# Performance work log

Hardware: AMD Instinct MI355X
Metric: run time of the kernel (lower is better)

The kernel has to match this reference:

```python
import jax, jax.numpy as jnp
import numpy as np

B, L, C = 4, 2048, 1024
H = 16
D = C // H  # 64
MAX_SCALE_MUL = float(np.log(100.0))


def setup_inputs() -> dict:
    key = jax.random.key(0)
    ks = jax.random.split(key, 8)
    x = jax.random.normal(ks[0], (B, L, C), dtype=jnp.float32)
    attn_bias = jax.random.normal(ks[1], (1, H, L, L), dtype=jnp.float32) * 0.02
    # nn.Linear(C, 3C, bias=False): weight [3C, C], init ~ U(-1/sqrt(C), 1/sqrt(C))
    lim = 1.0 / np.sqrt(C)
    W_qkv = jax.random.uniform(ks[2], (3 * C, C), minval=-lim, maxval=lim, dtype=jnp.float32)
    q_bias = jnp.zeros((C,), dtype=jnp.float32)
    v_bias = jnp.zeros((C,), dtype=jnp.float32)
    scale_mul_log = jnp.full((1, H, 1, 1), np.log(4.0), dtype=jnp.float32)
    W_proj = jax.random.uniform(ks[3], (C, C), minval=-lim, maxval=lim, dtype=jnp.float32)
    b_proj = jax.random.uniform(ks[4], (C,), minval=-lim, maxval=lim, dtype=jnp.float32)
    return {"x": x, "attn_bias": attn_bias, "W_qkv": W_qkv, "q_bias": q_bias,
            "v_bias": v_bias, "scale_mul_log": scale_mul_log,
            "W_proj": W_proj, "b_proj": b_proj}


def reference(x, attn_bias, W_qkv, q_bias, v_bias, scale_mul_log, W_proj, b_proj):
    Bc, Lc, Cc = x.shape
    qkv_bias = jnp.concatenate([q_bias, jnp.zeros_like(q_bias), v_bias])
    qkv = x @ W_qkv.T + qkv_bias                      # [B, L, 3C]
    qkv = qkv.reshape(Bc, Lc, 3, H, D)
    q, k, v = jnp.moveaxis(qkv, 2, 0)                 # each [B, L, H, D]
    q = jnp.swapaxes(q, 1, 2)                         # [B, H, L, D]
    k = jnp.swapaxes(k, 1, 2)
    v = jnp.swapaxes(v, 1, 2)
    # L2-norm cosine attention with learned per-head scale
    scale_mul = jnp.exp(jnp.minimum(scale_mul_log, MAX_SCALE_MUL))  # [1, H, 1, 1]
    q = q / jnp.linalg.norm(q, axis=-1, keepdims=True).clip(1e-12) * scale_mul
    k = k / jnp.linalg.norm(k, axis=-1, keepdims=True).clip(1e-12)
    attn = jnp.einsum('bhqd,bhkd->bhqk', q, k) + attn_bias
    attn = jax.nn.softmax(attn, axis=-1)
    out = jnp.einsum('bhqk,bhkd->bhqd', attn, v)      # [B, H, L, D]
    out = jnp.swapaxes(out, 1, 2).reshape(Bc, Lc, Cc)
    return out @ W_proj.T + b_proj
```

## Files before the change

### kernel.cpp

```cpp
#include <hip/hip_runtime.h>
#include <cstdint>
#include <cstddef>

#define BATCH 4
#define SEQ   2048
#define CMOD  1024
#define NH    16
#define DH    64
#define LOG100 4.6051701859880914f
#define LOG2E  1.4426950408889634f

typedef __attribute__((ext_vector_type(8))) short bf16x8;
typedef __attribute__((ext_vector_type(4))) float f32x4;
typedef __attribute__((ext_vector_type(16))) float f32x16;

__device__ __forceinline__ float u32lo_f(uint32_t u) {
    union { uint32_t i; float f; } x; x.i = u << 16; return x.f;
}
__device__ __forceinline__ float u32hi_f(uint32_t u) {
    union { uint32_t i; float f; } x; x.i = u & 0xFFFF0000u; return x.f;
}
__device__ __forceinline__ uint16_t f2bf(float f) {
    union { float f; uint32_t i; } x; x.f = f;
    uint32_t u = x.i;
    return (uint16_t)((u + 0x7FFFu + ((u >> 16) & 1u)) >> 16);
}
__device__ __forceinline__ float exp2_fast(float x) {
    float r; asm("v_exp_f32 %0, %1" : "=v"(r) : "v"(x)); return r;
}
__device__ __forceinline__ uint32_t cvt_pk_bf16(float lo, float hi) {
    uint32_t r;
    asm("v_cvt_pk_bf16_f32 %0, %1, %2" : "=v"(r) : "v"(lo), "v"(hi));
    return r;
}
__device__ __forceinline__ void p32swap(uint32_t& x, uint32_t& y) {
#if __has_builtin(__builtin_amdgcn_permlane32_swap)
    auto r = __builtin_amdgcn_permlane32_swap(x, y, false, false);
    x = r[0]; y = r[1];
#else
    asm volatile("v_permlane32_swap_b32 %0, %1\n\ts_nop 1" : "+v"(x), "+v"(y));
#endif
}

__device__ __forceinline__ void gload_lds16(const void* g, void* l) {
    __builtin_amdgcn_global_load_lds(
        (const __attribute__((address_space(1))) uint32_t*)g,
        (__attribute__((address_space(3))) uint32_t*)l,
        16, 0, 0);
}

__global__ __launch_bounds__(256) void cvt_kernel(const float* __restrict__ in,
                                                  uint16_t* __restrict__ out, int n) {
    int i = (blockIdx.x * 256 + threadIdx.x) * 4;
    if (i >= n) return;
    float4 f = *(const float4*)(in + i);
    ushort4 o;
    o.x = f2bf(f.x); o.y = f2bf(f.y); o.z = f2bf(f.z); o.w = f2bf(f.w);
    *(ushort4*)(out + i) = o;
}

__global__ __launch_bounds__(256) void gemm_bt_kernel(
    const uint16_t* __restrict__ A, const uint16_t* __restrict__ B,
    int M, int N, int K, int mode,
    uint16_t* __restrict__ qb, uint16_t* __restrict__ kb, uint16_t* __restrict__ vtb,
    const float* __restrict__ q_bias, const float* __restrict__ v_bias,
    const float* __restrict__ scale_mul_log,
    float* __restrict__ outp, const float* __restrict__ b_proj)
{
    __shared__ __align__(16) uint16_t As[128 * 32];
    __shared__ __align__(16) uint16_t Bs[128 * 32];
    const int t = threadIdx.x;
    const int wave = t >> 6, lane = t & 63;
    const int g = lane >> 4, c16 = lane & 15;
    const int m0 = blockIdx.x * 128, n0 = blockIdx.y * 128;
    const int wm = (wave >> 1) * 64, wn = (wave & 1) * 64;

    f32x4 acc[4][4];
#pragma unroll
    for (int mt = 0; mt < 4; mt++)
#pragma unroll
        for (int nt = 0; nt < 4; nt++) acc[mt][nt] = (f32x4){0.f, 0.f, 0.f, 0.f};

    for (int k0 = 0; k0 < K; k0 += 32) {
        __syncthreads();
#pragma unroll
        for (int i = 0; i < 2; i++) {
            int cc = i * 256 + t;
            int row = cc >> 2, col = (cc & 3) * 8;
            gload_lds16(A + (size_t)(m0 + row) * K + k0 + col, &As[cc * 8]);
            gload_lds16(B + (size_t)(n0 + row) * K + k0 + col, &Bs[cc * 8]);
        }
        __syncthreads();
        bf16x8 af[4], bfv[4];
#pragma unroll
        for (int mt = 0; mt < 4; mt++)
            af[mt] = *(const bf16x8*)&As[(wm + mt * 16 + c16) * 32 + g * 8];
#pragma unroll
        for (int nt = 0; nt < 4; nt++)
            bfv[nt] = *(const bf16x8*)&Bs[(wn + nt * 16 + c16) * 32 + g * 8];
#pragma unroll
        for (int mt = 0; mt < 4; mt++)
#pragma unroll
            for (int nt = 0; nt < 4; nt++)
                acc[mt][nt] = __builtin_amdgcn_mfma_f32_16x16x32_bf16(af[mt], bfv[nt], acc[mt][nt], 0, 0, 0);
    }

    if (mode == 0) {
        const int colbase = n0 + wn;
        const int tt = colbase >> 10;
        const int cc0 = colbase & 1023;
        const int hh = cc0 >> 6;
        float qmul = 1.0f;
        if (tt == 0) qmul = __expf(fminf(scale_mul_log[hh], LOG100)) * LOG2E;
#pragma unroll
        for (int mt = 0; mt < 4; mt++) {
            float vals[4][4];
            float n2[4] = {0.f, 0.f, 0.f, 0.f};
#pragma unroll
            for (int nt = 0; nt < 4; nt++) {
                const int ci = cc0 + nt * 16 + c16;
                float badd = 0.f;
                if (tt == 0) badd = q_bias[ci];
                else if (tt == 2) badd = v_bias[ci];
#pragma unroll
                for (int r = 0; r < 4; r++) {
                    float v = acc[mt][nt][r] + badd;
                    vals[nt][r] = v;
                    n2[r] += v * v;
                }
            }
            float rs[4];
            if (tt < 2) {
#pragma unroll
                for (int r = 0; r < 4; r++) {
                    float s = n2[r];
                    s += __shfl_xor(s, 1, 64);
                    s += __shfl_xor(s, 2, 64);
                    s += __shfl_xor(s, 4, 64);
                    s += __shfl_xor(s, 8, 64);
                    rs[r] = qmul / fmaxf(sqrtf(s), 1e-12f);
                }
            } else {
#pragma unroll
                for (int r = 0; r < 4; r++) rs[r] = 1.0f;
            }
#pragma unroll
            for (int nt = 0; nt < 4; nt++) {
                const int dd = (cc0 + nt * 16 + c16) & 63;
#pragma unroll
                for (int r = 0; r < 4; r++) {
                    const int row = m0 + wm + mt * 16 + g * 4 + r;
                    const int bb = row >> 11, ll = row & 2047;
                    const size_t bhx = (size_t)bb * NH + hh;
                    const uint16_t val = f2bf(vals[nt][r] * rs[r]);
                    if (tt < 2) {
                        size_t addr = ((bhx * 64 + (ll >> 5)) * 4 + (dd >> 4)) * 512
                                      + ((dd >> 3) & 1) * 256 + (ll & 31) * 8 + (dd & 7);
                        if (tt == 0) qb[addr] = val; else kb[addr] = val;
                    } else {
                        size_t addr = ((bhx * 64 + (ll >> 5)) * 4 + (dd >> 5) * 2 + ((ll >> 4) & 1)) * 512
                                      + (((ll >> 3) & 1) * 32 + (dd & 31)) * 8 + (ll & 7);
                        vtb[addr] = val;
                    }
                }
            }
        }
    } else {
#pragma unroll
        for (int mt = 0; mt < 4; mt++)
#pragma unroll
            for (int nt = 0; nt < 4; nt++)
#pragma unroll
                for (int r = 0; r < 4; r++) {
                    int row = m0 + wm + mt * 16 + g * 4 + r;
                    int col = n0 + wn + nt * 16 + c16;
                    outp[(size_t)row * N + col] = acc[mt][nt][r] + b_proj[col];
                }
    }
}

__global__ __launch_bounds__(256) void attn_kernel(
    const uint16_t* __restrict__ qfrag, const uint16_t* __restrict__ kfrag,
    const uint16_t* __restrict__ vfrag, const float* __restrict__ bias,
    uint16_t* __restrict__ ob)
{
    __shared__ __align__(16) uint16_t KsL[2 * 4 * 4 * 512];
    __shared__ __align__(16) uint16_t VsL[2 * 4 * 4 * 512];
    __shared__ __align__(16) uint2    Bsh[2 * 512];

    const int t = threadIdx.x;
    const int w = t >> 6, lane = t & 63;
    const int c32 = lane & 31, hi = lane >> 5;

    const int h = blockIdx.x >> 5;
    const int qt = blockIdx.x & 31;
    const int q0 = qt * 64;
    const size_t bh = (size_t)w * NH + h;

    bf16x8 qf[2][4];
#pragma unroll
    for (int qg = 0; qg < 2; qg++)
#pragma unroll
        for (int s = 0; s < 4; s++)
            qf[qg][s] = *(const bf16x8*)(qfrag +
                ((bh * 64 + (size_t)(qt * 2 + qg)) * 4 + s) * 512 + hi * 256 + c32 * 8);

    auto stage = [&](int tl, int buf) {
        const uint16_t* kp = kfrag + ((bh * 64 + (size_t)tl) * 4) * 512 + lane * 8;
        const uint16_t* vp = vfrag + ((bh * 64 + (size_t)tl) * 4) * 512 + lane * 8;
#pragma unroll
        for (int s = 0; s < 4; s++)
            gload_lds16(kp + s * 512, &KsL[((buf * 4 + w) * 4 + s) * 512 + lane * 8]);
#pragma unroll
        for (int s = 0; s < 4; s++)
            gload_lds16(vp + s * 512, &VsL[((buf * 4 + w) * 4 + s) * 512 + lane * 8]);
    };

    const int brow = t >> 2, kpart = t & 3;
    const float* bgl = bias + ((size_t)h * SEQ + q0 + brow) * SEQ + kpart * 8;
    const int u0 = kpart * 128 + (brow >> 5) * 64 + (brow & 31);

    auto writeBsh = [&](int buf, float4 a, float4 b) {
        Bsh[buf * 512 + u0] =
            make_uint2(cvt_pk_bf16(a.x * LOG2E, a.y * LOG2E),
                       cvt_pk_bf16(a.z * LOG2E, a.w * LOG2E));
        Bsh[buf * 512 + u0 + 32] =
            make_uint2(cvt_pk_bf16(b.x * LOG2E, b.y * LOG2E),
                       cvt_pk_bf16(b.z * LOG2E, b.w * LOG2E));
    };

    f32x16 accO[2][2];
#pragma unroll
    for (int qg = 0; qg < 2; qg++)
#pragma unroll
        for (int db = 0; db < 2; db++)
#pragma unroll
            for (int i = 0; i < 16; i++) accO[qg][db][i] = 0.f;
    float lrun[2] = {0.f, 0.f};

    float4 a0 = *(const float4*)(bgl);
    float4 a1 = *(const float4*)(bgl + 4);
    float4 br0 = *(const float4*)(bgl + 32);
    float4 br1 = *(const float4*)(bgl + 36);
    stage(0, 0);
    writeBsh(0, a0, a1);
    asm volatile("s_waitcnt lgkmcnt(0)" ::: "memory");
    __builtin_amdgcn_s_barrier();

    for (int it = 0; it < 64; ++it) {
        const int cur = it & 1;
        if (it < 63) {
            const int nb = cur ^ 1;
            writeBsh(nb, br0, br1);
            int n2 = it + 2; if (n2 > 63) n2 = 63;
            br0 = *(const float4*)(bgl + n2 * 32);
            br1 = *(const float4*)(bgl + n2 * 32 + 4);
            stage(it + 1, nb);
            asm volatile("s_waitcnt vmcnt(10)" ::: "memory");
        } else {
            asm volatile("s_waitcnt vmcnt(0)" ::: "memory");
        }

        bf16x8 kf[4], vf[4];
#pragma unroll
        for (int s = 0; s < 4; s++)
            kf[s] = *(const bf16x8*)&KsL[((cur * 4 + w) * 4 + s) * 512 + lane * 8];
#pragma unroll
        for (int s = 0; s < 4; s++)
            vf[s] = *(const bf16x8*)&VsL[((cur * 4 + w) * 4 + s) * 512 + lane * 8];

#pragma unroll
        for (int qg = 0; qg < 2; qg++) {
            f32x16 S;
#pragma unroll
            for (int i = 0; i < 16; i++) S[i] = 0.f;
            __builtin_amdgcn_s_setprio(1);
#pragma unroll
            for (int s = 0; s < 4; s++)
                S = __builtin_amdgcn_mfma_f32_32x32x16_bf16(kf[s], qf[qg][s], S, 0, 0, 0);
            __builtin_amdgcn_s_setprio(0);

            float p[16];
            float lp = 0.f;
#pragma unroll
            for (int tt = 0; tt < 4; tt++) {
                uint2 uu = Bsh[cur * 512 + tt * 128 + qg * 64 + hi * 32 + c32];
                p[tt * 4 + 0] = exp2_fast(S[tt * 4 + 0] + u32lo_f(uu.x));
                p[tt * 4 + 1] = exp2_fast(S[tt * 4 + 1] + u32hi_f(uu.x));
                p[tt * 4 + 2] = exp2_fast(S[tt * 4 + 2] + u32lo_f(uu.y));
                p[tt * 4 + 3] = exp2_fast(S[tt * 4 + 3] + u32hi_f(uu.y));
                lp += (p[tt * 4 + 0] + p[tt * 4 + 1]) + (p[tt * 4 + 2] + p[tt * 4 + 3]);
            }
            lrun[qg] += lp;

            bf16x8 pa[2];
#pragma unroll
            for (int cp = 0; cp < 2; cp++) {
                uint32_t X0 = cvt_pk_bf16(p[8 * cp + 0], p[8 * cp + 1]);
                uint32_t X1 = cvt_pk_bf16(p[8 * cp + 2], p[8 * cp + 3]);
                uint32_t Y0 = cvt_pk_bf16(p[8 * cp + 4], p[8 * cp + 5]);
                uint32_t Y1 = cvt_pk_bf16(p[8 * cp + 6], p[8 * cp + 7]);
                p32swap(X0, Y0);
                p32swap(X1, Y1);
                union { uint32_t u[4]; bf16x8 v; } pu;
                pu.u[0] = X0; pu.u[1] = X1; pu.u[2] = Y0; pu.u[3] = Y1;
                pa[cp] = pu.v;
            }

            __builtin_amdgcn_s_setprio(1);
#pragma unroll
            for (int c = 0; c < 2; c++)
#pragma unroll
                for (int db = 0; db < 2; db++)
                    accO[qg][db] = __builtin_amdgcn_mfma_f32_32x32x16_bf16(
                        pa[c], vf[db * 2 + c], accO[qg][db], 0, 0, 0);
            __builtin_amdgcn_s_setprio(0);
        }

        asm volatile("s_waitcnt lgkmcnt(0)" ::: "memory");
        __builtin_amdgcn_s_barrier();
    }

#pragma unroll
    for (int qg = 0; qg < 2; qg++) {
        float s = lrun[qg] + __shfl_xor(lrun[qg], 32, 64);
        float inv = 1.0f / s;
        float linv[16];
#pragma unroll
        for (int r = 0; r < 16; r++)
            linv[r] = __shfl(inv, (r & 3) + 8 * (r >> 2) + 4 * hi, 64);
#pragma unroll
        for (int r = 0; r < 16; r++) {
            int rowq = (r & 3) + 8 * (r >> 2) + 4 * hi;
            size_t rowbase = ((size_t)w * SEQ + q0 + qg * 32 + rowq) * CMOD + h * DH;
            ob[rowbase + c32]      = f2bf(accO[qg][0][r] * linv[r]);
            ob[rowbase + 32 + c32] = f2bf(accO[qg][1][r] * linv[r]);
        }
    }
}

extern "C" void kernel_launch(void* const* d_in, const int* in_sizes, int n_in,
                              void* d_out, int out_size, void* d_ws, size_t ws_size,
                              hipStream_t stream) {
    const float* x             = (const float*)d_in[0];
    const float* attn_bias     = (const float*)d_in[1];
    const float* W_qkv         = (const float*)d_in[2];
    const float* q_bias        = (const float*)d_in[3];
    const float* v_bias        = (const float*)d_in[4];
    const float* scale_mul_log = (const float*)d_in[5];
    const float* W_proj        = (const float*)d_in[6];
    const float* b_proj        = (const float*)d_in[7];
    float* out = (float*)d_out;

    uint8_t* ws = (uint8_t*)d_ws;
    size_t off = 0;
    auto alloc = [&](size_t bytes) { uint8_t* p = ws + off; off += (bytes + 255) & ~(size_t)255; return p; };
    uint16_t* xb     = (uint16_t*)alloc((size_t)8192 * 1024 * 2);
    uint16_t* wqkvb  = (uint16_t*)alloc((size_t)3072 * 1024 * 2);
    uint16_t* wprojb = (uint16_t*)alloc((size_t)1024 * 1024 * 2);
    uint16_t* qb     = (uint16_t*)alloc((size_t)BATCH * NH * SEQ * DH * 2);
    uint16_t* kb     = (uint16_t*)alloc((size_t)BATCH * NH * SEQ * DH * 2);
    uint16_t* vtb    = (uint16_t*)alloc((size_t)BATCH * NH * SEQ * DH * 2);
    uint16_t* ob     = (uint16_t*)alloc((size_t)BATCH * SEQ * CMOD * 2);
    (void)ws_size;

    cvt_kernel<<<8192, 256, 0, stream>>>(x, xb, 8388608);
    cvt_kernel<<<3072, 256, 0, stream>>>(W_qkv, wqkvb, 3145728);
    cvt_kernel<<<1024, 256, 0, stream>>>(W_proj, wprojb, 1048576);

    dim3 g1(64, 24);
    gemm_bt_kernel<<<g1, 256, 0, stream>>>(xb, wqkvb, 8192, 3072, 1024, 0,
                                           qb, kb, vtb, q_bias, v_bias, scale_mul_log,
                                           nullptr, nullptr);

    attn_kernel<<<512, 256, 0, stream>>>(qb, kb, vtb, attn_bias, ob);

    dim3 g3(64, 8);
    gemm_bt_kernel<<<g3, 256, 0, stream>>>(ob, wprojb, 8192, 1024, 1024, 1,
                                           nullptr, nullptr, nullptr, nullptr, nullptr, nullptr,
                                           out, b_proj);
}
```

Before: 304.8 us.

## Split attention work across eight waves per block, one query half each

Doubles the attention block to 512 threads. Each wave now handles one batch and a 32-row query half instead of both halves, and the K and V staging is split between the two groups of waves. The bias load per thread is halved, and explicit vmcnt/lgkmcnt waits and setprio are replaced with __syncthreads. The aim is more waves in flight to hide latency and less register use per wave, at the cost of larger blocks and coarser synchronisation.

```diff
diff --git a/kernel.cpp b/kernel.cpp
--- a/kernel.cpp
+++ b/kernel.cpp
@@ -179,7 +179,7 @@
     }
 }
 
-__global__ __launch_bounds__(256) void attn_kernel(
+__global__ __launch_bounds__(512, 4) void attn_kernel(
     const uint16_t* __restrict__ qfrag, const uint16_t* __restrict__ kfrag,
     const uint16_t* __restrict__ vfrag, const float* __restrict__ bias,
     uint16_t* __restrict__ ob)
@@ -189,153 +189,131 @@
     __shared__ __align__(16) uint2    Bsh[2 * 512];
 
     const int t = threadIdx.x;
-    const int w = t >> 6, lane = t & 63;
+    const int w8 = t >> 6, lane = t & 63;
+    const int b = w8 & 3, qhalf = w8 >> 2;
     const int c32 = lane & 31, hi = lane >> 5;
 
     const int h = blockIdx.x >> 5;
     const int qt = blockIdx.x & 31;
-    const int q0 = qt * 64;
-    const size_t bh = (size_t)w * NH + h;
-
-    bf16x8 qf[2][4];
-#pragma unroll
-    for (int qg = 0; qg < 2; qg++)
-#pragma unroll
-        for (int s = 0; s < 4; s++)
-            qf[qg][s] = *(const bf16x8*)(qfrag +
-                ((bh * 64 + (size_t)(qt * 2 + qg)) * 4 + s) * 512 + hi * 256 + c32 * 8);
+    const int q0w = qt * 64 + qhalf * 32;
+    const size_t bh = (size_t)b * NH + h;
+
+    bf16x8 qf[4];
+#pragma unroll
+    for (int s = 0; s < 4; s++)
+        qf[s] = *(const bf16x8*)(qfrag +
+            ((bh * 64 + (size_t)(qt * 2 + qhalf)) * 4 + s) * 512 + hi * 256 + c32 * 8);
 
     auto stage = [&](int tl, int buf) {
-        const uint16_t* kp = kfrag + ((bh * 64 + (size_t)tl) * 4) * 512 + lane * 8;
-        const uint16_t* vp = vfrag + ((bh * 64 + (size_t)tl) * 4) * 512 + lane * 8;
-#pragma unroll
-        for (int s = 0; s < 4; s++)
-            gload_lds16(kp + s * 512, &KsL[((buf * 4 + w) * 4 + s) * 512 + lane * 8]);
-#pragma unroll
-        for (int s = 0; s < 4; s++)
-            gload_lds16(vp + s * 512, &VsL[((buf * 4 + w) * 4 + s) * 512 + lane * 8]);
+        if (w8 < 4) {
+            const uint16_t* kp = kfrag + (((size_t)w8 * NH + h) * 64 + tl) * 4 * 512 + lane * 8;
+#pragma unroll
+            for (int s = 0; s < 4; s++)
+                gload_lds16(kp + s * 512, &KsL[((buf * 4 + w8) * 4 + s) * 512 + lane * 8]);
+        } else {
+            const int bb = w8 - 4;
+            const uint16_t* vp = vfrag + (((size_t)bb * NH + h) * 64 + tl) * 4 * 512 + lane * 8;
+#pragma unroll
+            for (int s = 0; s < 4; s++)
+                gload_lds16(vp + s * 512, &VsL[((buf * 4 + bb) * 4 + s) * 512 + lane * 8]);
+        }
     };
 
-    const int brow = t >> 2, kpart = t & 3;
-    const float* bgl = bias + ((size_t)h * SEQ + q0 + brow) * SEQ + kpart * 8;
-    const int u0 = kpart * 128 + (brow >> 5) * 64 + (brow & 31);
-
-    auto writeBsh = [&](int buf, float4 a, float4 b) {
+    const int brow = t >> 3, kch = t & 7;
+    const float* bgl = bias + ((size_t)h * SEQ + qt * 64 + brow) * SEQ + kch * 4;
+    const int u0 = (kch >> 1) * 128 + (brow >> 5) * 64 + (kch & 1) * 32 + (brow & 31);
+
+    auto writeBsh = [&](int buf, float4 a) {
         Bsh[buf * 512 + u0] =
             make_uint2(cvt_pk_bf16(a.x * LOG2E, a.y * LOG2E),
                        cvt_pk_bf16(a.z * LOG2E, a.w * LOG2E));
-        Bsh[buf * 512 + u0 + 32] =
-            make_uint2(cvt_pk_bf16(b.x * LOG2E, b.y * LOG2E),
-                       cvt_pk_bf16(b.z * LOG2E, b.w * LOG2E));
     };
 
-    f32x16 accO[2][2];
-#pragma unroll
-    for (int qg = 0; qg < 2; qg++)
-#pragma unroll
-        for (int db = 0; db < 2; db++)
-#pragma unroll
-            for (int i = 0; i < 16; i++) accO[qg][db][i] = 0.f;
-    float lrun[2] = {0.f, 0.f};
+    f32x16 accO[2];
+#pragma unroll
+    for (int db = 0; db < 2; db++)
+#pragma unroll
+        for (int i = 0; i < 16; i++) accO[db][i] = 0.f;
+    float lrun = 0.f;
 
     float4 a0 = *(const float4*)(bgl);
-    float4 a1 = *(const float4*)(bgl + 4);
     float4 br0 = *(const float4*)(bgl + 32);
-    float4 br1 = *(const float4*)(bgl + 36);
     stage(0, 0);
-    writeBsh(0, a0, a1);
-    asm volatile("s_waitcnt lgkmcnt(0)" ::: "memory");
-    __builtin_amdgcn_s_barrier();
+    writeBsh(0, a0);
+    __syncthreads();
 
     for (int it = 0; it < 64; ++it) {
         const int cur = it & 1;
         if (it < 63) {
             const int nb = cur ^ 1;
-            writeBsh(nb, br0, br1);
+            writeBsh(nb, br0);
             int n2 = it + 2; if (n2 > 63) n2 = 63;
             br0 = *(const float4*)(bgl + n2 * 32);
-            br1 = *(const float4*)(bgl + n2 * 32 + 4);
             stage(it + 1, nb);
-            asm volatile("s_waitcnt vmcnt(10)" ::: "memory");
-        } else {
-            asm volatile("s_waitcnt vmcnt(0)" ::: "memory");
-        }
-
-        bf16x8 kf[4], vf[4];
+        }
+
+        bf16x8 kf[4];
 #pragma unroll
         for (int s = 0; s < 4; s++)
-            kf[s] = *(const bf16x8*)&KsL[((cur * 4 + w) * 4 + s) * 512 + lane * 8];
+            kf[s] = *(const bf16x8*)&KsL[((cur * 4 + b) * 4 + s) * 512 + lane * 8];
+
+        f32x16 S;
+#pragma unroll
+        for (int i = 0; i < 16; i++) S[i] = 0.f;
 #pragma unroll
         for (int s = 0; s < 4; s++)
-            vf[s] = *(const bf16x8*)&VsL[((cur * 4 + w) * 4 + s) * 512 + lane * 8];
-
-#pragma unroll
-        for (int qg = 0; qg < 2; qg++) {
-            f32x16 S;
-#pragma unroll
-            for (int i = 0; i < 16; i++) S[i] = 0.f;
-            __builtin_amdgcn_s_setprio(1);
-#pragma unroll
-            for (int s = 0; s < 4; s++)
-                S = __builtin_amdgcn_mfma_f32_32x32x16_bf16(kf[s], qf[qg][s], S, 0, 0, 0);
-            __builtin_amdgcn_s_setprio(0);
-
-            float p[16];
-            float lp = 0.f;
-#pragma unroll
-            for (int tt = 0; tt < 4; tt++) {
-                uint2 uu = Bsh[cur * 512 + tt * 128 + qg * 64 + hi * 32 + c32];
-                p[tt * 4 + 0] = exp2_fast(S[tt * 4 + 0] + u32lo_f(uu.x));
-                p[tt * 4 + 1] = exp2_fast(S[tt * 4 + 1] + u32hi_f(uu.x));
-                p[tt * 4 + 2] = exp2_fast(S[tt * 4 + 2] + u32lo_f(uu.y));
-                p[tt * 4 + 3] = exp2_fast(S[tt * 4 + 3] + u32hi_f(uu.y));
-                lp += (p[tt * 4 + 0] + p[tt * 4 + 1]) + (p[tt * 4 + 2] + p[tt * 4 + 3]);
+            S = __builtin_amdgcn_mfma_f32_32x32x16_bf16(kf[s], qf[s], S, 0, 0, 0);
+
+        float p[16];
+        float lp = 0.f;
+#pragma unroll
+        for (int tt = 0; tt < 4; tt++) {
+            uint2 uu = Bsh[cur * 512 + tt * 128 + qhalf * 64 + hi * 32 + c32];
+            p[tt * 4 + 0] = exp2_fast(S[tt * 4 + 0] + u32lo_f(uu.x));
+            p[tt * 4 + 1] = exp2_fast(S[tt * 4 + 1] + u32hi_f(uu.x));
+            p[tt * 4 + 2] = exp2_fast(S[tt * 4 + 2] + u32lo_f(uu.y));
+            p[tt * 4 + 3] = exp2_fast(S[tt * 4 + 3] + u32hi_f(uu.y));
+            lp += (p[tt * 4 + 0] + p[tt * 4 + 1]) + (p[tt * 4 + 2] + p[tt * 4 + 3]);
+        }
+        lrun += lp;
+
+        bf16x8 pa[2];
+#pragma unroll
+        for (int cp = 0; cp < 2; cp++) {
+            uint32_t X0 = cvt_pk_bf16(p[8 * cp + 0], p[8 * cp + 1]);
+            uint32_t X1 = cvt_pk_bf16(p[8 * cp + 2], p[8 * cp + 3]);
+            uint32_t Y0 = cvt_pk_bf16(p[8 * cp + 4], p[8 * cp + 5]);
+            uint32_t Y1 = cvt_pk_bf16(p[8 * cp + 6], p[8 * cp + 7]);
+            p32swap(X0, Y0);
+            p32swap(X1, Y1);
+            union { uint32_t u[4]; bf16x8 v; } pu;
+            pu.u[0] = X0; pu.u[1] = X1; pu.u[2] = Y0; pu.u[3] = Y1;
+            pa[cp] = pu.v;
+        }
+
+#pragma unroll
+        for (int c = 0; c < 2; c++)
+#pragma unroll
+            for (int db = 0; db < 2; db++) {
+                bf16x8 vf = *(const bf16x8*)&VsL[((cur * 4 + b) * 4 + db * 2 + c) * 512 + lane * 8];
+                accO[db] = __builtin_amdgcn_mfma_f32_32x32x16_bf16(pa[c], vf, accO[db], 0, 0, 0);
             }
-            lrun[qg] += lp;
-
-            bf16x8 pa[2];
-#pragma unroll
-            for (int cp = 0; cp < 2; cp++) {
-                uint32_t X0 = cvt_pk_bf16(p[8 * cp + 0], p[8 * cp + 1]);
-                uint32_t X1 = cvt_pk_bf16(p[8 * cp + 2], p[8 * cp + 3]);
-                uint32_t Y0 = cvt_pk_bf16(p[8 * cp + 4], p[8 * cp + 5]);
-                uint32_t Y1 = cvt_pk_bf16(p[8 * cp + 6], p[8 * cp + 7]);
-                p32swap(X0, Y0);
-                p32swap(X1, Y1);
-                union { uint32_t u[4]; bf16x8 v; } pu;
-                pu.u[0] = X0; pu.u[1] = X1; pu.u[2] = Y0; pu.u[3] = Y1;
-                pa[cp] = pu.v;
-            }
-
-            __builtin_amdgcn_s_setprio(1);
-#pragma unroll
-            for (int c = 0; c < 2; c++)
-#pragma unroll
-                for (int db = 0; db < 2; db++)
-                    accO[qg][db] = __builtin_amdgcn_mfma_f32_32x32x16_bf16(
-                        pa[c], vf[db * 2 + c], accO[qg][db], 0, 0, 0);
-            __builtin_amdgcn_s_setprio(0);
-        }
-
-        asm volatile("s_waitcnt lgkmcnt(0)" ::: "memory");
-        __builtin_amdgcn_s_barrier();
+
+        __syncthreads();
     }
 
-#pragma unroll
-    for (int qg = 0; qg < 2; qg++) {
-        float s = lrun[qg] + __shfl_xor(lrun[qg], 32, 64);
-        float inv = 1.0f / s;
-        float linv[16];
-#pragma unroll
-        for (int r = 0; r < 16; r++)
-            linv[r] = __shfl(inv, (r & 3) + 8 * (r >> 2) + 4 * hi, 64);
-#pragma unroll
-        for (int r = 0; r < 16; r++) {
-            int rowq = (r & 3) + 8 * (r >> 2) + 4 * hi;
-            size_t rowbase = ((size_t)w * SEQ + q0 + qg * 32 + rowq) * CMOD + h * DH;
-            ob[rowbase + c32]      = f2bf(accO[qg][0][r] * linv[r]);
-            ob[rowbase + 32 + c32] = f2bf(accO[qg][1][r] * linv[r]);
-        }
+    float s = lrun + __shfl_xor(lrun, 32, 64);
+    float inv = 1.0f / s;
+    float linv[16];
+#pragma unroll
+    for (int r = 0; r < 16; r++)
+        linv[r] = __shfl(inv, (r & 3) + 8 * (r >> 2) + 4 * hi, 64);
+#pragma unroll
+    for (int r = 0; r < 16; r++) {
+        int rowq = (r & 3) + 8 * (r >> 2) + 4 * hi;
+        size_t rowbase = ((size_t)b * SEQ + q0w + rowq) * CMOD + h * DH;
+        ob[rowbase + c32]      = f2bf(accO[0][r] * linv[r]);
+        ob[rowbase + 32 + c32] = f2bf(accO[1][r] * linv[r]);
     }
 }
 
@@ -373,7 +351,7 @@
                                            qb, kb, vtb, q_bias, v_bias, scale_mul_log,
                                            nullptr, nullptr);
 
-    attn_kernel<<<512, 256, 0, stream>>>(qb, kb, vtb, attn_bias, ob);
+    attn_kernel<<<512, 512, 0, stream>>>(qb, kb, vtb, attn_bias, ob);
 
     dim3 g3(64, 8);
     gemm_bt_kernel<<<g3, 256, 0, stream>>>(ob, wprojb, 8192, 1024, 1024, 1,
```

New measurement: 284.8 us. -6.6%, faster.
